# Kernel tuning notes

Hardware: AMD Instinct MI355X
Metric: run time of the kernel (lower is better)

Reference implementation:

```python
import jax, jax.numpy as jnp
import numpy as np

# ---- static config (matches init_kwargs) ----
B = 32          # batch
CTX = 128       # context_dim
N_FRAMES = 128
N_SAMPLES = 32768
N_EVENTS = 16
CH = 256        # channels
WIN = 512       # window_size
HOP = WIN // 2  # 256
N_COEFFS = WIN // 2 + 1   # 257
TOTAL_COEFFS = N_COEFFS * 2  # 514


def _hann(n):
    # periodic Hann window (torch.hann_window default)
    i = jnp.arange(n, dtype=jnp.float32)
    return 0.5 * (1.0 - jnp.cos(2.0 * jnp.pi * i / n))


def _forward(param, times, noise, pos, proj_w, proj_b,
             w0, b0, w1, b1, w2, b2, w_out, b_out):
    # proj: [B, CTX] -> [B, CH]
    x = param @ proj_w.T + proj_b
    x = x[:, None, :] + pos                      # [B, N_FRAMES, CH] (pos broadcast)
    # LinearOutputStack: 3 hidden layers w/ leaky_relu(0.2), then output layer
    for w, b in ((w0, b0), (w1, b1), (w2, b2)):
        x = jax.nn.leaky_relu(x @ w.T + b, 0.2)
    x = x @ w_out.T + b_out                      # [B, N_FRAMES, 514]
    x = x.reshape(B, N_FRAMES, N_COEFFS, 2)
    mags = jnp.abs(x[..., 0])                    # [B, F, 257]
    phase = x[..., 1]
    # phase jitter: base phase of ones perturbed by uniform(-1,1) noise
    phase = 1.0 + phase * noise
    # mag/phase recomposition: per-frequency phase increment accumulated over frames
    freqs = jnp.linspace(0.0, 1.0, N_COEFFS)
    p = jnp.cumsum(phase * freqs * jnp.pi, axis=1)
    spec = mags * jnp.exp(1j * p)                # complex [B, F, 257]
    frames = jnp.fft.irfft(spec, n=WIN, axis=-1)  # [B, F, 512]
    frames = frames * _hann(WIN)
    total = (N_FRAMES - 1) * HOP + WIN
    idx = (jnp.arange(N_FRAMES) * HOP)[:, None] + jnp.arange(WIN)  # [F, 512]
    sig = jnp.zeros((B, total), frames.dtype).at[:, idx].add(frames)
    sig = sig[:, :N_SAMPLES]                     # [B, N_SAMPLES]
    # DiracScheduler (pre_sparse): upsample-with-holes frame-resolution diracs
    step = N_SAMPLES // N_FRAMES                 # 256
    up = jnp.zeros((B, N_EVENTS, N_SAMPLES), sig.dtype).at[:, :, ::step].set(times)
    # fft convolve event signal with dirac trains (zero-padded, linear conv)
    n2 = 2 * N_SAMPLES
    S = jnp.fft.rfft(sig, n=n2)[:, None, :]      # [B, 1, n2//2+1]
    T = jnp.fft.rfft(up, n=n2)                   # [B, E, n2//2+1]
    out = jnp.fft.irfft(S * T, n=n2)[..., :N_SAMPLES]
    return out                                   # [B, N_EVENTS, N_SAMPLES]


def setup_inputs() -> dict:
    key = jax.random.key(0)
    ks = jax.random.split(key, 16)
    s = 0.02
    param = jax.random.normal(ks[0], (B, CTX), jnp.float32)
    # sparse dirac times: one event position per (batch, event) at frame resolution
    posn = jax.random.randint(ks[1], (B, N_EVENTS), 0, N_FRAMES)
    amps = jax.random.uniform(ks[2], (B, N_EVENTS), jnp.float32, 0.1, 1.0)
    times = jax.nn.one_hot(posn, N_FRAMES, dtype=jnp.float32) * amps[..., None]
    noise = jax.random.uniform(ks[3], (B, N_FRAMES, N_COEFFS), jnp.float32, -1.0, 1.0)
    pos = jax.random.uniform(ks[4], (1, N_FRAMES, CH), jnp.float32, -0.01, 0.01)
    proj_w = jax.random.normal(ks[5], (CH, CTX), jnp.float32) * s
    proj_b = jnp.zeros((CH,), jnp.float32)
    w0 = jax.random.normal(ks[6], (CH, CH), jnp.float32) * s
    b0 = jnp.zeros((CH,), jnp.float32)
    w1 = jax.random.normal(ks[7], (CH, CH), jnp.float32) * s
    b1 = jnp.zeros((CH,), jnp.float32)
    w2 = jax.random.normal(ks[8], (CH, CH), jnp.float32) * s
    b2 = jnp.zeros((CH,), jnp.float32)
    w_out = jax.random.normal(ks[9], (TOTAL_COEFFS, CH), jnp.float32) * s
    b_out = jnp.zeros((TOTAL_COEFFS,), jnp.float32)
    return dict(param=param, times=times, noise=noise, pos=pos,
                proj_w=proj_w, proj_b=proj_b, w0=w0, b0=b0, w1=w1, b1=b1,
                w2=w2, b2=b2, w_out=w_out, b_out=b_out)


def reference(param, times, noise, pos, proj_w, proj_b,
              w0, b0, w1, b1, w2, b2, w_out, b_out):
    return _forward(param, times, noise, pos, proj_w, proj_b,
                    w0, b0, w1, b1, w2, b2, w_out, b_out)
```

## Files before the change

### kernel.cpp

```cpp
#include <hip/hip_runtime.h>
#include <cstddef>

typedef unsigned short u16;
typedef __bf16 bf16x8 __attribute__((ext_vector_type(8)));
typedef float f32x4 __attribute__((ext_vector_type(4)));

constexpr int B_   = 32;
constexpr int CTX_ = 128;
constexpr int NF_  = 128;
constexpr int NS_  = 32768;
constexpr int NE_  = 16;
constexpr int CH_  = 256;
constexpr int NC_  = 257;
constexpr int TC_  = 514;
constexpr int ROWS_ = B_ * NF_;
constexpr int CHUNK_ = 8;
constexpr int NCH_ = NF_ / CHUNK_;
constexpr int KE_ = 288;
constexpr int K3MLP_ = 768;
constexpr int K3IR_ = 896;
constexpr float PI_ = 3.14159265358979323846f;

__device__ __forceinline__ float lrelu(float v) { return v > 0.f ? v : 0.2f * v; }
__device__ __forceinline__ u16 f2bf(float x) {
    unsigned u = __float_as_uint(x);
    return (u16)((u + 0x7FFFu + ((u >> 16) & 1u)) >> 16);
}
__device__ __forceinline__ float bf2f(u16 h) { return __uint_as_float(((unsigned)h) << 16); }

__global__ __launch_bounds__(256) void prep_kernel(
    const float* __restrict__ param, const float* __restrict__ pw,
    const float* __restrict__ pb, const float* __restrict__ pos,
    const float* __restrict__ w1, const float* __restrict__ w2,
    const float* __restrict__ wo, const float* __restrict__ times,
    u16* __restrict__ Tt3, u16* __restrict__ W1_3, u16* __restrict__ W2_3,
    u16* __restrict__ WO_3, int* __restrict__ cnt, float2* __restrict__ taps,
    float* __restrict__ S)
{
    int blk = blockIdx.x;
    int tid = threadIdx.x;
    if (blk < 1792) {
        int idx = blk * 256 + tid;
        int z = idx / (256 * K3IR_);
        int r = idx - z * (256 * K3IR_);
        int n = r / K3IR_, col = r - n * K3IR_;
        u16 outv = 0;
        if (col < 864) {
            int seg = col / KE_;
            int j = col - seg * KE_;
            float val = 0.f;
            if (z == 0) {
                if (j < 129) {
                    int k = 2 * j;
                    float w = (k == 0 || k == 256) ? 1.f : 2.f;
                    int m = (k * n) & 511;
                    val = w * (1.f / 512.f) * cosf((float)m * (PI_ / 256.f));
                } else if (j < 258) {
                    int kk = 2 * (j - 129);
                    float w = (kk == 0 || kk == 256) ? 1.f : 2.f;
                    int m = (kk * n) & 511;
                    val = -w * (1.f / 512.f) * sinf((float)m * (PI_ / 256.f));
                }
            } else {
                if (j < 128) {
                    int k = 2 * j + 1;
                    int m = (k * n) & 511;
                    val = 2.f * (1.f / 512.f) * cosf((float)m * (PI_ / 256.f));
                } else if (j < 256) {
                    int kk = 2 * (j - 128) + 1;
                    int m = (kk * n) & 511;
                    val = -2.f * (1.f / 512.f) * sinf((float)m * (PI_ / 256.f));
                }
            }
            u16 h = f2bf(val);
            outv = (seg < 2) ? h : f2bf(val - bf2f(h));
        }
        Tt3[idx] = outv;
    } else if (blk < 2880) {
        int row = blk - 1792;
        int k = tid;
        float v;
        u16* p;
        if (row < 256) {
            v = w1[row * 256 + k];
            p = W1_3 + (size_t)row * K3MLP_;
        } else if (row < 512) {
            v = w2[(row - 256) * 256 + k];
            p = W2_3 + (size_t)(row - 256) * K3MLP_;
        } else {
            int n = row - 512;
            v = (n < TC_) ? wo[n * 256 + k] : 0.f;
            p = WO_3 + (size_t)n * K3MLP_;
        }
        u16 h = f2bf(v), lo = f2bf(v - bf2f(h));
        p[k] = h; p[256 + k] = h; p[512 + k] = lo;
    } else if (blk < 3392) {
        int be = blk - 2880;
        __shared__ int c;
        if (tid == 0) c = 0;
        __syncthreads();
        if (tid < NF_) {
            float v = times[(size_t)be * NF_ + tid];
            if (v != 0.f) {
                int slot = atomicAdd(&c, 1);
                taps[(size_t)be * NF_ + slot] = make_float2((float)tid, v);
            }
        }
        __syncthreads();
        if (tid == 0) cnt[be] = c;
    } else {
        int b = blk - 3392;
        int cth = tid;
        float v;
        if (b < 32) {
            const float* pr = param + b * CTX_;
            const float* wr = pw + cth * CTX_;
            float s = 0.f;
            #pragma unroll 4
            for (int j = 0; j < CTX_; ++j) s += pr[j] * wr[j];
            v = s + pb[cth];
        } else if (b < 160) {
            v = pos[(b - 32) * CH_ + cth];
        } else {
            v = 0.f;
        }
        S[b * CH_ + cth] = v;
    }
}

__global__ __launch_bounds__(256) void gemm2(
    const float* __restrict__ A, const float* __restrict__ Bm, float* __restrict__ C,
    int M, int N, int K, int lda, int ldb, int ldc)
{
    const int tid = threadIdx.x;
    const int tx = tid & 15, ty = tid >> 4;
    const int m0 = blockIdx.y * 64, n0 = blockIdx.x * 64;
    __shared__ __align__(16) float As[32][64];
    __shared__ __align__(16) float Bs[32][64];
    const int ar = tid & 63, akg = (tid >> 6) * 8;
    float4 ra0, ra1, rb0, rb1;
    auto loadA = [&](int kt) {
        const float* p = A + (size_t)(m0 + ar) * lda + kt + akg;
        ra0 = *(const float4*)p; ra1 = *(const float4*)(p + 4);
    };
    auto loadB = [&](int kt) {
        const float* p = Bm + (size_t)(n0 + ar) * ldb + kt + akg;
        rb0 = *(const float4*)p; rb1 = *(const float4*)(p + 4);
    };
    loadA(0); loadB(0);
    float acc[4][4] = {};
    for (int kt = 0; kt < K; kt += 32) {
        As[akg+0][ar] = ra0.x; As[akg+1][ar] = ra0.y; As[akg+2][ar] = ra0.z; As[akg+3][ar] = ra0.w;
        As[akg+4][ar] = ra1.x; As[akg+5][ar] = ra1.y; As[akg+6][ar] = ra1.z; As[akg+7][ar] = ra1.w;
        Bs[akg+0][ar] = rb0.x; Bs[akg+1][ar] = rb0.y; Bs[akg+2][ar] = rb0.z; Bs[akg+3][ar] = rb0.w;
        Bs[akg+4][ar] = rb1.x; Bs[akg+5][ar] = rb1.y; Bs[akg+6][ar] = rb1.z; Bs[akg+7][ar] = rb1.w;
        __syncthreads();
        if (kt + 32 < K) { loadA(kt + 32); loadB(kt + 32); }
        #pragma unroll
        for (int kk = 0; kk < 32; ++kk) {
            float4 av = *(const float4*)&As[kk][ty*4];
            float4 bv = *(const float4*)&Bs[kk][tx*4];
            float a4[4] = {av.x, av.y, av.z, av.w};
            float b4[4] = {bv.x, bv.y, bv.z, bv.w};
            #pragma unroll
            for (int i = 0; i < 4; ++i)
                #pragma unroll
                for (int j = 0; j < 4; ++j)
                    acc[i][j] += a4[i] * b4[j];
        }
        __syncthreads();
    }
    #pragma unroll
    for (int i = 0; i < 4; ++i)
        #pragma unroll
        for (int j = 0; j < 4; ++j)
            C[(size_t)(m0 + ty*4 + i) * ldc + n0 + tx*4 + j] = acc[i][j];
}

__global__ void fuse1_kernel(const float* __restrict__ YP, const float* __restrict__ b0,
                             u16* __restrict__ H3) {
    int idx = blockIdx.x * 256 + threadIdx.x;
    int c = idx & 255;
    int row = idx >> 8;
    int b = row >> 7, f = row & 127;
    float v = lrelu(YP[b * CH_ + c] + YP[(32 + f) * CH_ + c] + b0[c]);
    u16 h = f2bf(v), lo = f2bf(v - bf2f(h));
    u16* p = H3 + (size_t)row * K3MLP_;
    p[c] = h; p[256 + c] = lo; p[512 + c] = h;
}

template<int EPI, int K3>
__global__ __launch_bounds__(256) void mfgemm(
    const u16* __restrict__ A3, const u16* __restrict__ B3,
    const float* __restrict__ bias, void* __restrict__ Cout,
    int N, int lda, int ldb, int ldc,
    size_t sAz, size_t sBz, size_t sCz)
{
    A3 += (size_t)blockIdx.z * sAz;
    B3 += (size_t)blockIdx.z * sBz;
    const int tid = threadIdx.x;
    const int m0 = blockIdx.y * 64, n0 = blockIdx.x * 64;
    __shared__ __align__(16) u16 Als[2 * 64 * 64];
    __shared__ __align__(16) u16 Bls[2 * 64 * 64];
    const int sr = tid >> 2;
    const int sc = (tid & 3) * 16;
    const u16* ga = A3 + (size_t)(m0 + sr) * lda + sc;
    const u16* gb = B3 + (size_t)(n0 + sr) * ldb + sc;
    const int xr = (sr & 7) << 4;
    const int lo0 = sr * 128 + ((sc * 2) ^ xr);
    const int lo1 = sr * 128 + ((sc * 2 + 16) ^ xr);
    const int wv = tid >> 6, lane = tid & 63;
    const int wr = (wv >> 1) * 32, wc = (wv & 1) * 32;
    const int lr = lane & 15;
    const int lkb = (lane >> 4) * 16;
    const int xf = (lr & 7) << 4;
    const int ra0 = (wr + lr) * 128, ra1 = (wr + 16 + lr) * 128;
    const int rb0 = (wc + lr) * 128, rb1 = (wc + 16 + lr) * 128;
    f32x4 acc00 = {0.f, 0.f, 0.f, 0.f}, acc01 = acc00, acc10 = acc00, acc11 = acc00;

    uint4 pa0, pa1, pb0, pb1;
    uint4 qa0, qa1, qb0, qb1;
    auto loadP = [&](int kt) {
        pa0 = *(const uint4*)(ga + kt); pa1 = *(const uint4*)(ga + kt + 8);
        pb0 = *(const uint4*)(gb + kt); pb1 = *(const uint4*)(gb + kt + 8);
    };
    auto loadQ = [&](int kt) {
        qa0 = *(const uint4*)(ga + kt); qa1 = *(const uint4*)(ga + kt + 8);
        qb0 = *(const uint4*)(gb + kt); qb1 = *(const uint4*)(gb + kt + 8);
    };
    auto compute = [&](int p) {
        const char* pa = (const char*)Als + p * 8192;
        const char* pb = (const char*)Bls + p * 8192;
        #pragma unroll
        for (int s = 0; s < 2; ++s) {
            int kb = (s * 64 + lkb) ^ xf;
            bf16x8 a0 = *(const bf16x8*)(pa + ra0 + kb);
            bf16x8 a1 = *(const bf16x8*)(pa + ra1 + kb);
            bf16x8 b0 = *(const bf16x8*)(pb + rb0 + kb);
            bf16x8 b1 = *(const bf16x8*)(pb + rb1 + kb);
            acc00 = __builtin_amdgcn_mfma_f32_16x16x32_bf16(a0, b0, acc00, 0, 0, 0);
            acc01 = __builtin_amdgcn_mfma_f32_16x16x32_bf16(a0, b1, acc01, 0, 0, 0);
            acc10 = __builtin_amdgcn_mfma_f32_16x16x32_bf16(a1, b0, acc10, 0, 0, 0);
            acc11 = __builtin_amdgcn_mfma_f32_16x16x32_bf16(a1, b1, acc11, 0, 0, 0);
        }
    };
    loadP(0);
    loadQ(64);
    int p = 0;
    #pragma unroll
    for (int kt = 0; kt < K3; kt += 128) {
        {
            char* ab = (char*)Als + p * 8192;
            char* bb = (char*)Bls + p * 8192;
            *(uint4*)(ab + lo0) = pa0; *(uint4*)(ab + lo1) = pa1;
            *(uint4*)(bb + lo0) = pb0; *(uint4*)(bb + lo1) = pb1;
            __syncthreads();
            if (kt + 128 < K3) loadP(kt + 128);
            compute(p);
            p ^= 1;
        }
        {
            char* ab = (char*)Als + p * 8192;
            char* bb = (char*)Bls + p * 8192;
            *(uint4*)(ab + lo0) = qa0; *(uint4*)(ab + lo1) = qa1;
            *(uint4*)(bb + lo0) = qb0; *(uint4*)(bb + lo1) = qb1;
            __syncthreads();
            if (kt + 192 < K3) loadQ(kt + 192);
            compute(p);
            p ^= 1;
        }
    }
    const int er = (lane >> 4) * 4;
    const int ec = lane & 15;
    auto emit = [&](const f32x4& A, int mi, int ni) {
        #pragma unroll
        for (int r = 0; r < 4; ++r) {
            int m = m0 + wr + mi * 16 + er + r;
            int n = n0 + wc + ni * 16 + ec;
            float v = A[r];
            if (EPI == 0) {
                v = lrelu(v + bias[n]);
                u16 h = f2bf(v), lo = f2bf(v - bf2f(h));
                u16* p2 = (u16*)Cout + (size_t)m * ldc + n;
                p2[0] = h; p2[256] = lo; p2[512] = h;
            } else if (EPI == 1) {
                if (n < N) ((float*)Cout)[(size_t)m * ldc + n] = v + bias[n];
            } else {
                float* cf = (float*)Cout + (size_t)blockIdx.z * sCz;
                cf[(size_t)m * ldc + n] = v;
            }
        }
    };
    emit(acc00, 0, 0); emit(acc01, 0, 1); emit(acc10, 1, 0); emit(acc11, 1, 1);
}

__global__ void scan1_kernel(const float* __restrict__ raw, const float* __restrict__ noise,
                             double* __restrict__ sums) {
    int b = blockIdx.x, c = blockIdx.y;
    int k = threadIdx.x;
    if (k >= NC_) return;
    float kf = (float)k * (PI_ / 256.f);
    double s = 0.0;
    #pragma unroll
    for (int j = 0; j < CHUNK_; ++j) {
        int row = b * NF_ + c * CHUNK_ + j;
        float2 v = *(const float2*)(raw + (size_t)row * TC_ + 2 * k);
        float d = (1.f + v.y * noise[(size_t)row * NC_ + k]) * kf;
        s += (double)d;
    }
    sums[((size_t)(b * NCH_ + c)) * NC_ + k] = s;
}

__global__ void scan2_kernel(const float* __restrict__ raw, const float* __restrict__ noise,
                             const double* __restrict__ sums,
                             u16* __restrict__ AB3e, u16* __restrict__ AB3o) {
    int b = blockIdx.x, c = blockIdx.y;
    int k = threadIdx.x;
    if (k >= NC_) {
        int t = k - NC_;
        for (int idx = t; idx < 250; idx += 63) {
            int col;
            u16* base;
            if (idx < 122) {
                col = (idx < 90) ? ((idx / 30) * KE_ + 258 + (idx % 30)) : (864 + (idx - 90));
                base = AB3e;
            } else {
                int u = idx - 122;
                col = (u < 96) ? ((u / 32) * KE_ + 256 + (u % 32)) : (864 + (u - 96));
                base = AB3o;
            }
            for (int j = 0; j < CHUNK_; ++j)
                base[(size_t)(b * NF_ + c * CHUNK_ + j) * K3IR_ + col] = 0;
        }
        return;
    }
    double p = 0.0;
    for (int cc = 0; cc < c; ++cc)
        p += sums[((size_t)(b * NCH_ + cc)) * NC_ + k];
    float kf = (float)k * (PI_ / 256.f);
    int half = k >> 1;
    bool even = (k & 1) == 0;
    int ccol = half;
    int scol = even ? (129 + half) : (128 + half);
    u16* dst = even ? AB3e : AB3o;
    for (int j = 0; j < CHUNK_; ++j) {
        int row = b * NF_ + c * CHUNK_ + j;
        float2 v = *(const float2*)(raw + (size_t)row * TC_ + 2 * k);
        float d = (1.f + v.y * noise[(size_t)row * NC_ + k]) * kf;
        p += (double)d;
        float m = fabsf(v.x);
        float sn, cs;
        sincosf((float)p, &sn, &cs);
        float a = m * cs, bb = m * sn;
        u16* pr = dst + (size_t)row * K3IR_;
        u16 ha = f2bf(a), la = f2bf(a - bf2f(ha));
        pr[ccol] = ha; pr[KE_ + ccol] = la; pr[2 * KE_ + ccol] = ha;
        u16 hb = f2bf(bb), lb = f2bf(bb - bf2f(hb));
        pr[scol] = hb; pr[KE_ + scol] = lb; pr[2 * KE_ + scol] = hb;
    }
}

__global__ __launch_bounds__(256) void conv2_kernel(const float* __restrict__ E,
                                                    const float* __restrict__ O,
                                                    const int* __restrict__ cnt,
                                                    const float2* __restrict__ taps,
                                                    float* __restrict__ out) {
    int be = blockIdx.y;
    int b = be >> 4;
    int n = cnt[be];
    int t = blockIdx.x * 2048 + (int)threadIdx.x * 8;
    int r0 = t & 255;
    float hr[8], hr2[8];
    #pragma unroll
    for (int j = 0; j < 8; ++j) {
        float cj = cosf((float)(r0 + j) * (PI_ / 256.f));
        hr[j]  = 0.5f - 0.5f * cj;
        hr2[j] = 0.5f + 0.5f * cj;
    }
    float acc[8] = {};
    for (int i = 0; i < n; ++i) {
        float2 ka = taps[(size_t)be * NF_ + i];
        int s0 = t - ((int)ka.x << 8);
        if (s0 < 0) continue;
        float amp = ka.y;
        int q = s0 >> 8;
        size_t row = (size_t)(b * NF_ + q) * 256 + r0;
        float4 e0 = *(const float4*)(E + row);
        float4 e1 = *(const float4*)(E + row + 4);
        float4 o0 = *(const float4*)(O + row);
        float4 o1 = *(const float4*)(O + row + 4);
        float sv[8];
        sv[0] = hr[0] * (e0.x + o0.x); sv[1] = hr[1] * (e0.y + o0.y);
        sv[2] = hr[2] * (e0.z + o0.z); sv[3] = hr[3] * (e0.w + o0.w);
        sv[4] = hr[4] * (e1.x + o1.x); sv[5] = hr[5] * (e1.y + o1.y);
        sv[6] = hr[6] * (e1.z + o1.z); sv[7] = hr[7] * (e1.w + o1.w);
        if (q > 0) {
            float4 pe0 = *(const float4*)(E + row - 256);
            float4 pe1 = *(const float4*)(E + row - 252);
            float4 po0 = *(const float4*)(O + row - 256);
            float4 po1 = *(const float4*)(O + row - 252);
            sv[0] += hr2[0] * (pe0.x - po0.x); sv[1] += hr2[1] * (pe0.y - po0.y);
            sv[2] += hr2[2] * (pe0.z - po0.z); sv[3] += hr2[3] * (pe0.w - po0.w);
            sv[4] += hr2[4] * (pe1.x - po1.x); sv[5] += hr2[5] * (pe1.y - po1.y);
            sv[6] += hr2[6] * (pe1.z - po1.z); sv[7] += hr2[7] * (pe1.w - po1.w);
        }
        #pragma unroll
        for (int j = 0; j < 8; ++j) acc[j] += amp * sv[j];
    }
    float* op = out + (size_t)be * NS_ + t;
    float4 w0v = make_float4(acc[0], acc[1], acc[2], acc[3]);
    float4 w1v = make_float4(acc[4], acc[5], acc[6], acc[7]);
    *(float4*)op = w0v;
    *(float4*)(op + 4) = w1v;
}

extern "C" void kernel_launch(void* const* d_in, const int* in_sizes, int n_in,
                              void* d_out, int out_size, void* d_ws, size_t ws_size,
                              hipStream_t stream) {
    const float* param  = (const float*)d_in[0];
    const float* times  = (const float*)d_in[1];
    const float* noise  = (const float*)d_in[2];
    const float* pos    = (const float*)d_in[3];
    const float* proj_w = (const float*)d_in[4];
    const float* proj_b = (const float*)d_in[5];
    const float* w0 = (const float*)d_in[6];
    const float* b0 = (const float*)d_in[7];
    const float* w1 = (const float*)d_in[8];
    const float* b1 = (const float*)d_in[9];
    const float* w2 = (const float*)d_in[10];
    const float* b2 = (const float*)d_in[11];
    const float* w_out = (const float*)d_in[12];
    const float* b_out = (const float*)d_in[13];
    float* out = (float*)d_out;
    float* ws = (float*)d_ws;

    constexpr size_t S_F    = 192 * 256;
    constexpr size_t YP_F   = 192 * 256;
    constexpr size_t H3_F   = (size_t)ROWS_ * K3MLP_ / 2;
    constexpr size_t W3_F   = (size_t)256 * K3MLP_ / 2;
    constexpr size_t WO3_F  = (size_t)576 * K3MLP_ / 2;
    constexpr size_t RAW_F  = (size_t)ROWS_ * TC_;
    constexpr size_t AB3_F  = 2 * (size_t)ROWS_ * K3IR_ / 2;
    constexpr size_t TT3_F  = 2 * (size_t)256 * K3IR_ / 2;
    constexpr size_t EO_F   = 2 * (size_t)ROWS_ * 256;
    constexpr size_t SUMS_F = (size_t)B_ * NCH_ * NC_ * 2;

    size_t cur = 0;
    float* S    = ws + cur;                 cur += S_F;
    float* YP   = ws + cur;                 cur += YP_F;
    u16*  H1_3  = (u16*)(ws + cur);         cur += H3_F;
    u16*  H2_3  = (u16*)(ws + cur);         cur += H3_F;
    u16*  H3_3  = (u16*)(ws + cur);         cur += H3_F;
    u16*  W1_3  = (u16*)(ws + cur);         cur += W3_F;
    u16*  W2_3  = (u16*)(ws + cur);         cur += W3_F;
    u16*  WO_3  = (u16*)(ws + cur);         cur += WO3_F;
    float* RAW  = ws + cur;                 cur += RAW_F;
    u16*  AB3   = (u16*)(ws + cur);         cur += AB3_F;
    u16*  AB3e  = AB3;
    u16*  AB3o  = AB3 + (size_t)ROWS_ * K3IR_;
    u16*  Tt3   = (u16*)(ws + cur);         cur += TT3_F;
    float* EO   = ws + cur;                 cur += EO_F;
    double* SUMS = (double*)(ws + cur);     cur += SUMS_F;
    int*   CNT  = (int*)(ws + cur);         cur += 512;
    float2* TAPS = (float2*)(ws + cur);

    prep_kernel<<<3584, 256, 0, stream>>>(param, proj_w, proj_b, pos, w1, w2, w_out,
                                          times, Tt3, W1_3, W2_3, WO_3, CNT, TAPS, S);
    gemm2<<<dim3(4, 3, 1), 256, 0, stream>>>(S, w0, YP, 192, CH_, CH_, CH_, CH_, CH_);
    fuse1_kernel<<<ROWS_ * CH_ / 256, 256, 0, stream>>>(YP, b0, H1_3);
    mfgemm<0, K3MLP_><<<dim3(4, 64, 1), 256, 0, stream>>>(H1_3, W1_3, b1, H2_3, 256,
                                                          K3MLP_, K3MLP_, K3MLP_, 0, 0, 0);
    mfgemm<0, K3MLP_><<<dim3(4, 64, 1), 256, 0, stream>>>(H2_3, W2_3, b2, H3_3, 256,
                                                          K3MLP_, K3MLP_, K3MLP_, 0, 0, 0);
    mfgemm<1, K3MLP_><<<dim3(9, 64, 1), 256, 0, stream>>>(H3_3, WO_3, b_out, RAW, TC_,
                                                          K3MLP_, K3MLP_, TC_, 0, 0, 0);
    dim3 gS(B_, NCH_);
    scan1_kernel<<<gS, 320, 0, stream>>>(RAW, noise, SUMS);
    scan2_kernel<<<gS, 320, 0, stream>>>(RAW, noise, SUMS, AB3e, AB3o);
    mfgemm<2, K3IR_><<<dim3(4, 64, 2), 256, 0, stream>>>(AB3, Tt3, nullptr, EO, 256,
                                                         K3IR_, K3IR_, 256,
                                                         (size_t)ROWS_ * K3IR_,
                                                         (size_t)256 * K3IR_,
                                                         (size_t)ROWS_ * 256);
    dim3 gC(NS_ / 2048, B_ * NE_);
    conv2_kernel<<<gC, 256, 0, stream>>>(EO, EO + (size_t)ROWS_ * 256, CNT, TAPS, out);
}
```

Measured before the change: 107.8 us.

## Fold first-layer GEMM into prep kernel and shrink MFMA GEMM tiles to 32x64

The separate fp32 gemm2 launch is removed. The projection-then-w0 product for each batch row and the pos-times-w0 product for each frame are now computed inside prep_kernel as U and V, which removes one kernel launch and its serialization. The bf16 MFMA GEMM now uses 128-thread blocks with 32x64 output tiles, doubling the grid so more blocks are spread across CUs. In exchange, each B tile is reused by fewer rows, and prep_kernel now runs serial dot products over 256-length rows.

```diff
diff --git a/kernel.cpp b/kernel.cpp
--- a/kernel.cpp
+++ b/kernel.cpp
@@ -31,11 +31,12 @@
 __global__ __launch_bounds__(256) void prep_kernel(
     const float* __restrict__ param, const float* __restrict__ pw,
     const float* __restrict__ pb, const float* __restrict__ pos,
-    const float* __restrict__ w1, const float* __restrict__ w2,
-    const float* __restrict__ wo, const float* __restrict__ times,
+    const float* __restrict__ w0, const float* __restrict__ w1,
+    const float* __restrict__ w2, const float* __restrict__ wo,
+    const float* __restrict__ times,
     u16* __restrict__ Tt3, u16* __restrict__ W1_3, u16* __restrict__ W2_3,
     u16* __restrict__ WO_3, int* __restrict__ cnt, float2* __restrict__ taps,
-    float* __restrict__ S)
+    float* __restrict__ U, float* __restrict__ V)
 {
     int blk = blockIdx.x;
     int tid = threadIdx.x;
@@ -108,89 +109,50 @@
         }
         __syncthreads();
         if (tid == 0) cnt[be] = c;
-    } else {
+    } else if (blk < 3424) {
         int b = blk - 3392;
-        int cth = tid;
-        float v;
-        if (b < 32) {
+        __shared__ float ly[256];
+        {
             const float* pr = param + b * CTX_;
-            const float* wr = pw + cth * CTX_;
+            const float* wr = pw + tid * CTX_;
             float s = 0.f;
             #pragma unroll 4
             for (int j = 0; j < CTX_; ++j) s += pr[j] * wr[j];
-            v = s + pb[cth];
-        } else if (b < 160) {
-            v = pos[(b - 32) * CH_ + cth];
-        } else {
-            v = 0.f;
-        }
-        S[b * CH_ + cth] = v;
-    }
-}
-
-__global__ __launch_bounds__(256) void gemm2(
-    const float* __restrict__ A, const float* __restrict__ Bm, float* __restrict__ C,
-    int M, int N, int K, int lda, int ldb, int ldc)
-{
-    const int tid = threadIdx.x;
-    const int tx = tid & 15, ty = tid >> 4;
-    const int m0 = blockIdx.y * 64, n0 = blockIdx.x * 64;
-    __shared__ __align__(16) float As[32][64];
-    __shared__ __align__(16) float Bs[32][64];
-    const int ar = tid & 63, akg = (tid >> 6) * 8;
-    float4 ra0, ra1, rb0, rb1;
-    auto loadA = [&](int kt) {
-        const float* p = A + (size_t)(m0 + ar) * lda + kt + akg;
-        ra0 = *(const float4*)p; ra1 = *(const float4*)(p + 4);
-    };
-    auto loadB = [&](int kt) {
-        const float* p = Bm + (size_t)(n0 + ar) * ldb + kt + akg;
-        rb0 = *(const float4*)p; rb1 = *(const float4*)(p + 4);
-    };
-    loadA(0); loadB(0);
-    float acc[4][4] = {};
-    for (int kt = 0; kt < K; kt += 32) {
-        As[akg+0][ar] = ra0.x; As[akg+1][ar] = ra0.y; As[akg+2][ar] = ra0.z; As[akg+3][ar] = ra0.w;
-        As[akg+4][ar] = ra1.x; As[akg+5][ar] = ra1.y; As[akg+6][ar] = ra1.z; As[akg+7][ar] = ra1.w;
-        Bs[akg+0][ar] = rb0.x; Bs[akg+1][ar] = rb0.y; Bs[akg+2][ar] = rb0.z; Bs[akg+3][ar] = rb0.w;
-        Bs[akg+4][ar] = rb1.x; Bs[akg+5][ar] = rb1.y; Bs[akg+6][ar] = rb1.z; Bs[akg+7][ar] = rb1.w;
+            ly[tid] = s + pb[tid];
+        }
         __syncthreads();
-        if (kt + 32 < K) { loadA(kt + 32); loadB(kt + 32); }
-        #pragma unroll
-        for (int kk = 0; kk < 32; ++kk) {
-            float4 av = *(const float4*)&As[kk][ty*4];
-            float4 bv = *(const float4*)&Bs[kk][tx*4];
-            float a4[4] = {av.x, av.y, av.z, av.w};
-            float b4[4] = {bv.x, bv.y, bv.z, bv.w};
-            #pragma unroll
-            for (int i = 0; i < 4; ++i)
-                #pragma unroll
-                for (int j = 0; j < 4; ++j)
-                    acc[i][j] += a4[i] * b4[j];
-        }
-        __syncthreads();
-    }
-    #pragma unroll
-    for (int i = 0; i < 4; ++i)
-        #pragma unroll
-        for (int j = 0; j < 4; ++j)
-            C[(size_t)(m0 + ty*4 + i) * ldc + n0 + tx*4 + j] = acc[i][j];
-}
-
-__global__ void fuse1_kernel(const float* __restrict__ YP, const float* __restrict__ b0,
-                             u16* __restrict__ H3) {
+        {
+            const float* wn = w0 + tid * CH_;
+            float s = 0.f;
+            #pragma unroll 4
+            for (int c2 = 0; c2 < CH_; ++c2) s += ly[c2] * wn[c2];
+            U[b * CH_ + tid] = s;
+        }
+    } else {
+        int f = blk - 3424;
+        const float* pf = pos + f * CH_;
+        const float* wn = w0 + tid * CH_;
+        float s = 0.f;
+        #pragma unroll 4
+        for (int c2 = 0; c2 < CH_; ++c2) s += pf[c2] * wn[c2];
+        V[f * CH_ + tid] = s;
+    }
+}
+
+__global__ void fuse1_kernel(const float* __restrict__ U, const float* __restrict__ V,
+                             const float* __restrict__ b0, u16* __restrict__ H3) {
     int idx = blockIdx.x * 256 + threadIdx.x;
     int c = idx & 255;
     int row = idx >> 8;
     int b = row >> 7, f = row & 127;
-    float v = lrelu(YP[b * CH_ + c] + YP[(32 + f) * CH_ + c] + b0[c]);
+    float v = lrelu(U[b * CH_ + c] + V[f * CH_ + c] + b0[c]);
     u16 h = f2bf(v), lo = f2bf(v - bf2f(h));
     u16* p = H3 + (size_t)row * K3MLP_;
     p[c] = h; p[256 + c] = lo; p[512 + c] = h;
 }
 
 template<int EPI, int K3>
-__global__ __launch_bounds__(256) void mfgemm(
+__global__ __launch_bounds__(128) void mfgemm(
     const u16* __restrict__ A3, const u16* __restrict__ B3,
     const float* __restrict__ bias, void* __restrict__ Cout,
     int N, int lda, int ldb, int ldc,
@@ -199,83 +161,88 @@
     A3 += (size_t)blockIdx.z * sAz;
     B3 += (size_t)blockIdx.z * sBz;
     const int tid = threadIdx.x;
-    const int m0 = blockIdx.y * 64, n0 = blockIdx.x * 64;
-    __shared__ __align__(16) u16 Als[2 * 64 * 64];
+    const int m0 = blockIdx.y * 32, n0 = blockIdx.x * 64;
+    __shared__ __align__(16) u16 Als[2 * 32 * 64];
     __shared__ __align__(16) u16 Bls[2 * 64 * 64];
     const int sr = tid >> 2;
     const int sc = (tid & 3) * 16;
-    const u16* ga = A3 + (size_t)(m0 + sr) * lda + sc;
-    const u16* gb = B3 + (size_t)(n0 + sr) * ldb + sc;
+    const u16* ga  = A3 + (size_t)(m0 + sr) * lda + sc;
+    const u16* gb0 = B3 + (size_t)(n0 + sr) * ldb + sc;
+    const u16* gb1 = B3 + (size_t)(n0 + 32 + sr) * ldb + sc;
     const int xr = (sr & 7) << 4;
-    const int lo0 = sr * 128 + ((sc * 2) ^ xr);
-    const int lo1 = sr * 128 + ((sc * 2 + 16) ^ xr);
+    const int loA0 = sr * 128 + ((sc * 2) ^ xr);
+    const int loA1 = sr * 128 + ((sc * 2 + 16) ^ xr);
+    const int loB0 = sr * 128 + ((sc * 2) ^ xr);
+    const int loB1 = sr * 128 + ((sc * 2 + 16) ^ xr);
+    const int loB2 = (sr + 32) * 128 + ((sc * 2) ^ xr);
+    const int loB3 = (sr + 32) * 128 + ((sc * 2 + 16) ^ xr);
     const int wv = tid >> 6, lane = tid & 63;
-    const int wr = (wv >> 1) * 32, wc = (wv & 1) * 32;
+    const int wc = wv * 32;
     const int lr = lane & 15;
     const int lkb = (lane >> 4) * 16;
     const int xf = (lr & 7) << 4;
-    const int ra0 = (wr + lr) * 128, ra1 = (wr + 16 + lr) * 128;
-    const int rb0 = (wc + lr) * 128, rb1 = (wc + 16 + lr) * 128;
+    const int raf0 = lr * 128, raf1 = (16 + lr) * 128;
+    const int rbf0 = (wc + lr) * 128, rbf1 = (wc + 16 + lr) * 128;
     f32x4 acc00 = {0.f, 0.f, 0.f, 0.f}, acc01 = acc00, acc10 = acc00, acc11 = acc00;
 
-    uint4 pa0, pa1, pb0, pb1;
-    uint4 qa0, qa1, qb0, qb1;
+    uint4 pa0, pa1, pb0, pb1, pb2, pb3;
+    uint4 qa0, qa1, qb0, qb1, qb2, qb3;
     auto loadP = [&](int kt) {
-        pa0 = *(const uint4*)(ga + kt); pa1 = *(const uint4*)(ga + kt + 8);
-        pb0 = *(const uint4*)(gb + kt); pb1 = *(const uint4*)(gb + kt + 8);
+        pa0 = *(const uint4*)(ga + kt);  pa1 = *(const uint4*)(ga + kt + 8);
+        pb0 = *(const uint4*)(gb0 + kt); pb1 = *(const uint4*)(gb0 + kt + 8);
+        pb2 = *(const uint4*)(gb1 + kt); pb3 = *(const uint4*)(gb1 + kt + 8);
     };
     auto loadQ = [&](int kt) {
-        qa0 = *(const uint4*)(ga + kt); qa1 = *(const uint4*)(ga + kt + 8);
-        qb0 = *(const uint4*)(gb + kt); qb1 = *(const uint4*)(gb + kt + 8);
+        qa0 = *(const uint4*)(ga + kt);  qa1 = *(const uint4*)(ga + kt + 8);
+        qb0 = *(const uint4*)(gb0 + kt); qb1 = *(const uint4*)(gb0 + kt + 8);
+        qb2 = *(const uint4*)(gb1 + kt); qb3 = *(const uint4*)(gb1 + kt + 8);
     };
     auto compute = [&](int p) {
-        const char* pa = (const char*)Als + p * 8192;
+        const char* pa = (const char*)Als + p * 4096;
         const char* pb = (const char*)Bls + p * 8192;
         #pragma unroll
         for (int s = 0; s < 2; ++s) {
             int kb = (s * 64 + lkb) ^ xf;
-            bf16x8 a0 = *(const bf16x8*)(pa + ra0 + kb);
-            bf16x8 a1 = *(const bf16x8*)(pa + ra1 + kb);
-            bf16x8 b0 = *(const bf16x8*)(pb + rb0 + kb);
-            bf16x8 b1 = *(const bf16x8*)(pb + rb1 + kb);
+            bf16x8 a0 = *(const bf16x8*)(pa + raf0 + kb);
+            bf16x8 a1 = *(const bf16x8*)(pa + raf1 + kb);
+            bf16x8 b0 = *(const bf16x8*)(pb + rbf0 + kb);
+            bf16x8 b1 = *(const bf16x8*)(pb + rbf1 + kb);
             acc00 = __builtin_amdgcn_mfma_f32_16x16x32_bf16(a0, b0, acc00, 0, 0, 0);
             acc01 = __builtin_amdgcn_mfma_f32_16x16x32_bf16(a0, b1, acc01, 0, 0, 0);
             acc10 = __builtin_amdgcn_mfma_f32_16x16x32_bf16(a1, b0, acc10, 0, 0, 0);
             acc11 = __builtin_amdgcn_mfma_f32_16x16x32_bf16(a1, b1, acc11, 0, 0, 0);
         }
+    };
+    auto stage = [&](int p, const uint4& a0, const uint4& a1, const uint4& b0,
+                     const uint4& b1, const uint4& b2, const uint4& b3) {
+        char* ab = (char*)Als + p * 4096;
+        char* bb = (char*)Bls + p * 8192;
+        *(uint4*)(ab + loA0) = a0; *(uint4*)(ab + loA1) = a1;
+        *(uint4*)(bb + loB0) = b0; *(uint4*)(bb + loB1) = b1;
+        *(uint4*)(bb + loB2) = b2; *(uint4*)(bb + loB3) = b3;
     };
     loadP(0);
     loadQ(64);
     int p = 0;
     #pragma unroll
     for (int kt = 0; kt < K3; kt += 128) {
-        {
-            char* ab = (char*)Als + p * 8192;
-            char* bb = (char*)Bls + p * 8192;
-            *(uint4*)(ab + lo0) = pa0; *(uint4*)(ab + lo1) = pa1;
-            *(uint4*)(bb + lo0) = pb0; *(uint4*)(bb + lo1) = pb1;
-            __syncthreads();
-            if (kt + 128 < K3) loadP(kt + 128);
-            compute(p);
-            p ^= 1;
-        }
-        {
-            char* ab = (char*)Als + p * 8192;
-            char* bb = (char*)Bls + p * 8192;
-            *(uint4*)(ab + lo0) = qa0; *(uint4*)(ab + lo1) = qa1;
-            *(uint4*)(bb + lo0) = qb0; *(uint4*)(bb + lo1) = qb1;
-            __syncthreads();
-            if (kt + 192 < K3) loadQ(kt + 192);
-            compute(p);
-            p ^= 1;
-        }
+        stage(p, pa0, pa1, pb0, pb1, pb2, pb3);
+        __syncthreads();
+        if (kt + 128 < K3) loadP(kt + 128);
+        compute(p);
+        p ^= 1;
+        stage(p, qa0, qa1, qb0, qb1, qb2, qb3);
+        __syncthreads();
+        if (kt + 192 < K3) loadQ(kt + 192);
+        compute(p);
+        p ^= 1;
     }
     const int er = (lane >> 4) * 4;
     const int ec = lane & 15;
     auto emit = [&](const f32x4& A, int mi, int ni) {
         #pragma unroll
         for (int r = 0; r < 4; ++r) {
-            int m = m0 + wr + mi * 16 + er + r;
+            int m = m0 + mi * 16 + er + r;
             int n = n0 + wc + ni * 16 + ec;
             float v = A[r];
             if (EPI == 0) {
@@ -408,10 +375,8 @@
         for (int j = 0; j < 8; ++j) acc[j] += amp * sv[j];
     }
     float* op = out + (size_t)be * NS_ + t;
-    float4 w0v = make_float4(acc[0], acc[1], acc[2], acc[3]);
-    float4 w1v = make_float4(acc[4], acc[5], acc[6], acc[7]);
-    *(float4*)op = w0v;
-    *(float4*)(op + 4) = w1v;
+    *(float4*)op = make_float4(acc[0], acc[1], acc[2], acc[3]);
+    *(float4*)(op + 4) = make_float4(acc[4], acc[5], acc[6], acc[7]);
 }
 
 extern "C" void kernel_launch(void* const* d_in, const int* in_sizes, int n_in,
@@ -434,8 +399,8 @@
     float* out = (float*)d_out;
     float* ws = (float*)d_ws;
 
-    constexpr size_t S_F    = 192 * 256;
-    constexpr size_t YP_F   = 192 * 256;
+    constexpr size_t U_F    = 32 * 256;
+    constexpr size_t V_F    = 128 * 256;
     constexpr size_t H3_F   = (size_t)ROWS_ * K3MLP_ / 2;
     constexpr size_t W3_F   = (size_t)256 * K3MLP_ / 2;
     constexpr size_t WO3_F  = (size_t)576 * K3MLP_ / 2;
@@ -446,8 +411,8 @@
     constexpr size_t SUMS_F = (size_t)B_ * NCH_ * NC_ * 2;
 
     size_t cur = 0;
-    float* S    = ws + cur;                 cur += S_F;
-    float* YP   = ws + cur;                 cur += YP_F;
+    float* U    = ws + cur;                 cur += U_F;
+    float* V    = ws + cur;                 cur += V_F;
     u16*  H1_3  = (u16*)(ws + cur);         cur += H3_F;
     u16*  H2_3  = (u16*)(ws + cur);         cur += H3_F;
     u16*  H3_3  = (u16*)(ws + cur);         cur += H3_F;
@@ -464,24 +429,23 @@
     int*   CNT  = (int*)(ws + cur);         cur += 512;
     float2* TAPS = (float2*)(ws + cur);
 
-    prep_kernel<<<3584, 256, 0, stream>>>(param, proj_w, proj_b, pos, w1, w2, w_out,
-                                          times, Tt3, W1_3, W2_3, WO_3, CNT, TAPS, S);
-    gemm2<<<dim3(4, 3, 1), 256, 0, stream>>>(S, w0, YP, 192, CH_, CH_, CH_, CH_, CH_);
-    fuse1_kernel<<<ROWS_ * CH_ / 256, 256, 0, stream>>>(YP, b0, H1_3);
-    mfgemm<0, K3MLP_><<<dim3(4, 64, 1), 256, 0, stream>>>(H1_3, W1_3, b1, H2_3, 256,
-                                                          K3MLP_, K3MLP_, K3MLP_, 0, 0, 0);
-    mfgemm<0, K3MLP_><<<dim3(4, 64, 1), 256, 0, stream>>>(H2_3, W2_3, b2, H3_3, 256,
-                                                          K3MLP_, K3MLP_, K3MLP_, 0, 0, 0);
-    mfgemm<1, K3MLP_><<<dim3(9, 64, 1), 256, 0, stream>>>(H3_3, WO_3, b_out, RAW, TC_,
-                                                          K3MLP_, K3MLP_, TC_, 0, 0, 0);
+    prep_kernel<<<3552, 256, 0, stream>>>(param, proj_w, proj_b, pos, w0, w1, w2, w_out,
+                                          times, Tt3, W1_3, W2_3, WO_3, CNT, TAPS, U, V);
+    fuse1_kernel<<<ROWS_ * CH_ / 256, 256, 0, stream>>>(U, V, b0, H1_3);
+    mfgemm<0, K3MLP_><<<dim3(4, 128, 1), 128, 0, stream>>>(H1_3, W1_3, b1, H2_3, 256,
+                                                           K3MLP_, K3MLP_, K3MLP_, 0, 0, 0);
+    mfgemm<0, K3MLP_><<<dim3(4, 128, 1), 128, 0, stream>>>(H2_3, W2_3, b2, H3_3, 256,
+                                                           K3MLP_, K3MLP_, K3MLP_, 0, 0, 0);
+    mfgemm<1, K3MLP_><<<dim3(9, 128, 1), 128, 0, stream>>>(H3_3, WO_3, b_out, RAW, TC_,
+                                                           K3MLP_, K3MLP_, TC_, 0, 0, 0);
     dim3 gS(B_, NCH_);
     scan1_kernel<<<gS, 320, 0, stream>>>(RAW, noise, SUMS);
     scan2_kernel<<<gS, 320, 0, stream>>>(RAW, noise, SUMS, AB3e, AB3o);
-    mfgemm<2, K3IR_><<<dim3(4, 64, 2), 256, 0, stream>>>(AB3, Tt3, nullptr, EO, 256,
-                                                         K3IR_, K3IR_, 256,
-                                                         (size_t)ROWS_ * K3IR_,
-                                                         (size_t)256 * K3IR_,
-                                                         (size_t)ROWS_ * 256);
+    mfgemm<2, K3IR_><<<dim3(4, 128, 2), 128, 0, stream>>>(AB3, Tt3, nullptr, EO, 256,
+                                                          K3IR_, K3IR_, 256,
+                                                          (size_t)ROWS_ * K3IR_,
+                                                          (size_t)256 * K3IR_,
+                                                          (size_t)ROWS_ * 256);
     dim3 gC(NS_ / 2048, B_ * NE_);
     conv2_kernel<<<gC, 256, 0, stream>>>(EO, EO + (size_t)ROWS_ * 256, CNT, TAPS, out);
 }
```

Result: no change. 106.4 us (-1.3%).
